# Kernel tuning notes

Measured on AMD Instinct MI355X. Metric: run time of the kernel, lower is better.

Reference implementation:

```python
import jax, jax.numpy as jnp
import numpy as np

# norse default LIFParameters / LIParameters constants
DT = 1e-3
TAU_SYN_INV = 200.0
TAU_MEM_INV = 100.0
V_LEAK = 0.0
V_TH = 1.0
V_RESET = 0.0
ALPHA = 100.0  # superspike surrogate-gradient slope


@jax.custom_vjp
def superspike(x):
    return (x > 0).astype(x.dtype)

def _ss_fwd(x):
    return (x > 0).astype(x.dtype), x

def _ss_bwd(x, g):
    return (g / (ALPHA * jnp.abs(x) + 1.0) ** 2,)

superspike.defvjp(_ss_fwd, _ss_bwd)


def lif_step(state, inp):
    """norse lif_feed_forward_step: decay v/i, spike on old current, then inject input."""
    v, i = state
    v_dec = v + DT * TAU_MEM_INV * ((V_LEAK - v) + i)
    i_dec = i - DT * TAU_SYN_INV * i
    z = superspike(v_dec - V_TH)
    v_new = (1.0 - z) * v_dec + z * V_RESET
    return z, (v_new, i_dec + inp)


def li_step(state, inp):
    """norse li_feed_forward_step: leaky integrator, output is the membrane voltage."""
    v, i = state
    v_new = v + DT * TAU_MEM_INV * ((V_LEAK - v) + i)
    i_new = i - DT * TAU_SYN_INV * i + inp
    return v_new, (v_new, i_new)


def setup_inputs() -> dict:
    key = jax.random.key(0)
    ks = jax.random.split(key, 5)
    B = 65536
    x = jax.random.normal(ks[0], (B, 1, 10, 10), dtype=jnp.float32)
    conv_w = jax.random.normal(ks[1], (2, 1, 4, 4), dtype=jnp.float32) * 0.3
    conv_b = jax.random.normal(ks[2], (2,), dtype=jnp.float32) * 0.1
    fc_w = jax.random.normal(ks[3], (10, 72), dtype=jnp.float32) * 0.1
    fc_b = jax.random.normal(ks[4], (10,), dtype=jnp.float32) * 0.1
    return {"x": x, "conv_w": conv_w, "conv_b": conv_b, "fc_w": fc_w, "fc_b": fc_b, "num_steps": 64}


def reference(x, conv_w, conv_b, fc_w, fc_b, num_steps):
    B = x.shape[0]
    out_dim = fc_w.shape[0]
    # static input: conv(x) identical at every step, hoist out of the time loop
    g = jax.lax.conv_general_dilated(
        x, conv_w, (1, 1), "VALID",
        dimension_numbers=("NCHW", "OIHW", "NCHW"),
    ) + conv_b[None, :, None, None]  # [B,2,7,7]

    def pool(z):  # MaxPool2d(kernel=2, stride=1), VALID
        return jax.lax.reduce_window(
            z, -jnp.inf, jax.lax.max, (1, 1, 2, 2), (1, 1, 1, 1), "VALID")

    s_lif0 = (jnp.zeros_like(g), jnp.zeros_like(g))                 # [B,2,7,7]
    s_li1_0 = (jnp.zeros((B, 2, 6, 6), x.dtype), jnp.zeros((B, 2, 6, 6), x.dtype))
    s_li2_0 = (jnp.zeros((B, out_dim), x.dtype), jnp.zeros((B, out_dim), x.dtype))

    def step(carry, _):
        s_lif, s1, s2 = carry
        z, s_lif = lif_step(s_lif, g)          # spikes [B,2,7,7]
        z = pool(z)                            # [B,2,6,6]
        z, s1 = li_step(s1, z)                 # LI voltage [B,2,6,6]
        z = z.reshape(B, -1)                   # [B,72]
        z = z @ fc_w.T + fc_b                  # [B,10]
        v, s2 = li_step(s2, z)                 # readout voltage [B,10]
        return (s_lif, s1, s2), None

    (s_lif, s1, s2), _ = jax.lax.scan(step, (s_lif0, s_li1_0, s_li2_0), None, length=num_steps)
    return s2[0]  # final readout membrane voltage [B, output_size]
```

## Files before the change

### kernel.cpp

```cpp
#include <hip/hip_runtime.h>

#define TMAX 64

__global__ __launch_bounds__(256) void snn_fused(
    const float* __restrict__ x,
    const float* __restrict__ conv_w,
    const float* __restrict__ conv_b,
    const float* __restrict__ fc_w,
    const float* __restrict__ fc_b,
    const int*   __restrict__ nsteps,
    float*       __restrict__ out,
    int B)
{
    __shared__ double d_F[TMAX];
    __shared__ float  s_r[TMAX];
    __shared__ float  s_tab[8][256];
    __shared__ float  s_fcw[720];
    __shared__ float  s_fcb[16];
    __shared__ float  s_cb;

    const int tid = threadIdx.x;
    int T = nsteps[0];
    if (T > TMAX) T = TMAX;
    if (T < 0) T = 0;

    if (tid < TMAX) {
        double p9 = 1.0, p8 = 1.0;
        for (int k = 0; k < tid; ++k) { p9 *= 0.9; p8 *= 0.8; }
        d_F[tid] = p9 - p8;
    }
    for (int idx = tid; idx < 720; idx += 256) s_fcw[idx] = fc_w[idx];
    if (tid < 10) s_fcb[tid] = fc_b[tid];
    __syncthreads();

    if (tid < TMAX) {
        double r = 0.0;
        if (tid < T) {
            const int n = T - 1 - tid;
            for (int u = 0; u <= n; ++u) r += d_F[n - u] * d_F[u];
        }
        s_r[tid] = (float)r;
    }
    if (tid == 0) {
        double cb = 0.0;
        for (int m = 0; m < T; ++m) cb += d_F[m];
        s_cb = (float)cb;
    }
    __syncthreads();

    {
        const int v8 = tid;
        #pragma unroll
        for (int k = 0; k < 8; ++k) {
            float ssum = 0.f;
            #pragma unroll
            for (int bb = 0; bb < 8; ++bb)
                if ((v8 >> bb) & 1) ssum += s_r[k * 8 + bb];
            s_tab[k][v8] = ssum;
        }
    }
    __syncthreads();

    const float cbsum = s_cb;

    const int gt = blockIdx.x * 256 + tid;
    const int b = gt >> 1;
    const int c = gt & 1;
    if (b >= B) return;

    const float* xb = x + b * 100;

    float wc[16];
    {
        const float4* wq = reinterpret_cast<const float4*>(conv_w + c * 16);
        #pragma unroll
        for (int k = 0; k < 4; ++k) {
            float4 t = wq[k];
            wc[4*k+0] = t.x; wc[4*k+1] = t.y; wc[4*k+2] = t.z; wc[4*k+3] = t.w;
        }
    }
    const float cbias = conv_b[c];

    float outacc[10];
    #pragma unroll
    for (int o = 0; o < 10; ++o) outacc[o] = 0.f;

    unsigned int plo[7], phi[7];
    #pragma unroll
    for (int xx = 0; xx < 7; ++xx) { plo[xx] = 0u; phi[xx] = 0u; }

    const int tlo = T < 32 ? T : 32;
    const int thi = T > 32 ? (T - 32) : 0;

    for (int y = 0; y < 7; ++y) {
        float gg7[7];
        #pragma unroll
        for (int xx = 0; xx < 7; ++xx) gg7[xx] = 0.f;
        #pragma unroll
        for (int ky = 0; ky < 4; ++ky) {
            float xrow[10];
            const float2* q = reinterpret_cast<const float2*>(xb + (y + ky) * 10);
            #pragma unroll
            for (int k = 0; k < 5; ++k) { float2 t = q[k]; xrow[2*k] = t.x; xrow[2*k+1] = t.y; }
            #pragma unroll
            for (int xx = 0; xx < 7; ++xx) {
                float a = gg7[xx];
                #pragma unroll
                for (int kx = 0; kx < 4; ++kx)
                    a = __fadd_rn(a, __fmul_rn(wc[ky*4 + kx], xrow[xx + kx]));
                gg7[xx] = a;
            }
        }
        #pragma unroll
        for (int xx = 0; xx < 7; ++xx) gg7[xx] = __fadd_rn(gg7[xx], cbias);

        float v[7], ii[7];
        unsigned int mlo[7], mhi[7];
        #pragma unroll
        for (int xx = 0; xx < 7; ++xx) { v[xx] = 0.f; ii[xx] = 0.f; mlo[xx] = 0u; mhi[xx] = 0u; }

        #pragma unroll 4
        for (int t = 0; t < tlo; ++t) {
            const unsigned int bit = 1u << t;
            #pragma unroll
            for (int xx = 0; xx < 7; ++xx) {
                const float imv  = __fsub_rn(ii[xx], v[xx]);
                const float vdec = __fadd_rn(v[xx], __fmul_rn(0.1f, imv));
                const float idec = __fsub_rn(ii[xx], __fmul_rn(0.2f, ii[xx]));
                const bool  sp   = vdec > 1.0f;
                v[xx]  = sp ? 0.f : vdec;
                ii[xx] = __fadd_rn(idec, gg7[xx]);
                if (sp) mlo[xx] |= bit;
            }
        }
        #pragma unroll 4
        for (int t = 0; t < thi; ++t) {
            const unsigned int bit = 1u << t;
            #pragma unroll
            for (int xx = 0; xx < 7; ++xx) {
                const float imv  = __fsub_rn(ii[xx], v[xx]);
                const float vdec = __fadd_rn(v[xx], __fmul_rn(0.1f, imv));
                const float idec = __fsub_rn(ii[xx], __fmul_rn(0.2f, ii[xx]));
                const bool  sp   = vdec > 1.0f;
                v[xx]  = sp ? 0.f : vdec;
                ii[xx] = __fadd_rn(idec, gg7[xx]);
                if (sp) mhi[xx] |= bit;
            }
        }

        if (y > 0) {
            const int jbase = c * 36 + (y - 1) * 6;
            #pragma unroll
            for (int px = 0; px < 6; ++px) {
                const unsigned int pl = plo[px] | plo[px+1] | mlo[px] | mlo[px+1];
                const unsigned int ph = phi[px] | phi[px+1] | mhi[px] | mhi[px+1];
                float a = s_tab[0][pl & 255] + s_tab[1][(pl >> 8) & 255]
                        + s_tab[2][(pl >> 16) & 255] + s_tab[3][pl >> 24]
                        + s_tab[4][ph & 255] + s_tab[5][(ph >> 8) & 255]
                        + s_tab[6][(ph >> 16) & 255] + s_tab[7][ph >> 24];
                const int j = jbase + px;
                #pragma unroll
                for (int o = 0; o < 10; ++o)
                    outacc[o] = fmaf(s_fcw[o * 72 + j], a, outacc[o]);
            }
        }
        #pragma unroll
        for (int xx = 0; xx < 7; ++xx) { plo[xx] = mlo[xx]; phi[xx] = mhi[xx]; }
    }

    #pragma unroll
    for (int o = 0; o < 10; ++o) {
        float tot = outacc[o] + __shfl_xor(outacc[o], 1);
        tot = fmaf(cbsum, s_fcb[o], tot);
        if (c == 0) out[b * 10 + o] = tot;
    }
}

extern "C" void kernel_launch(void* const* d_in, const int* in_sizes, int n_in,
                              void* d_out, int out_size, void* d_ws, size_t ws_size,
                              hipStream_t stream) {
    const float* x      = (const float*)d_in[0];
    const float* conv_w = (const float*)d_in[1];
    const float* conv_b = (const float*)d_in[2];
    const float* fc_w   = (const float*)d_in[3];
    const float* fc_b   = (const float*)d_in[4];
    const int*   nsteps = (const int*)d_in[5];
    float* outp = (float*)d_out;

    const int B = in_sizes[0] / 100;
    const int total = 2 * B;
    const int block = 256;
    const int grid = (total + block - 1) / block;
    snn_fused<<<grid, block, 0, stream>>>(x, conv_w, conv_b, fc_w, fc_b, nsteps, outp, B);
}
```

Measured before the change: 96.45 us.

## Split rows across two threads per channel and use carry-shift spike masks

Each (batch, channel) pair is now handled by two threads that each simulate four overlapping rows, doubling thread count at the cost of recomputing one shared row. Spike bitmasks are built with inline asm that shifts in the compare carry, removing per-step bit construction. The pooled-weight lookup table is reversed to match the new bit order. The partial sums are reduced across four lanes with shuffles.

Result: faster. 91.05 us (-5.6%).

```diff
diff --git a/kernel.cpp b/kernel.cpp
--- a/kernel.cpp
+++ b/kernel.cpp
@@ -14,6 +14,7 @@
 {
     __shared__ double d_F[TMAX];
     __shared__ float  s_r[TMAX];
+    __shared__ float  s_rb[TMAX];
     __shared__ float  s_tab[8][256];
     __shared__ float  s_fcw[720];
     __shared__ float  s_fcb[16];
@@ -23,6 +24,8 @@
     int T = nsteps[0];
     if (T > TMAX) T = TMAX;
     if (T < 0) T = 0;
+    const int tlo = T < 32 ? T : 32;
+    const int thi = T > 32 ? (T - 32) : 0;
 
     if (tid < TMAX) {
         double p9 = 1.0, p8 = 1.0;
@@ -48,6 +51,14 @@
     }
     __syncthreads();
 
+    if (tid < 32) {
+        s_rb[tid] = (tid < tlo) ? s_r[tlo - 1 - tid] : 0.f;
+    } else if (tid < 64) {
+        const int p = tid - 32;
+        s_rb[tid] = (p < thi) ? s_r[tlo + thi - 1 - p] : 0.f;
+    }
+    __syncthreads();
+
     {
         const int v8 = tid;
         #pragma unroll
@@ -55,7 +66,7 @@
             float ssum = 0.f;
             #pragma unroll
             for (int bb = 0; bb < 8; ++bb)
-                if ((v8 >> bb) & 1) ssum += s_r[k * 8 + bb];
+                if ((v8 >> bb) & 1) ssum += s_rb[k * 8 + bb];
             s_tab[k][v8] = ssum;
         }
     }
@@ -64,8 +75,9 @@
     const float cbsum = s_cb;
 
     const int gt = blockIdx.x * 256 + tid;
-    const int b = gt >> 1;
-    const int c = gt & 1;
+    const int h = gt & 1;
+    const int c = (gt >> 1) & 1;
+    const int b = gt >> 2;
     if (b >= B) return;
 
     const float* xb = x + b * 100;
@@ -86,13 +98,13 @@
     for (int o = 0; o < 10; ++o) outacc[o] = 0.f;
 
     unsigned int plo[7], phi[7];
-    #pragma unroll
-    for (int xx = 0; xx < 7; ++xx) { plo[xx] = 0u; phi[xx] = 0u; }
-
-    const int tlo = T < 32 ? T : 32;
-    const int thi = T > 32 ? (T - 32) : 0;
-
-    for (int y = 0; y < 7; ++y) {
+    float fzero = 0.0f;
+
+    const int ybase = 3 * h;
+
+    for (int r = 0; r < 4; ++r) {
+        const int y = ybase + r;
+
         float gg7[7];
         #pragma unroll
         for (int xx = 0; xx < 7; ++xx) gg7[xx] = 0.f;
@@ -121,35 +133,44 @@
 
         #pragma unroll 4
         for (int t = 0; t < tlo; ++t) {
-            const unsigned int bit = 1u << t;
             #pragma unroll
             for (int xx = 0; xx < 7; ++xx) {
                 const float imv  = __fsub_rn(ii[xx], v[xx]);
                 const float vdec = __fadd_rn(v[xx], __fmul_rn(0.1f, imv));
                 const float idec = __fsub_rn(ii[xx], __fmul_rn(0.2f, ii[xx]));
-                const bool  sp   = vdec > 1.0f;
-                v[xx]  = sp ? 0.f : vdec;
+                float vnew;
+                asm("v_cmp_lt_f32 vcc, 1.0, %[vd]\n\t"
+                    "v_cndmask_b32 %[vn], %[vd], %[vz], vcc\n\t"
+                    "v_addc_co_u32 %[mm], vcc, %[mm], %[mm], vcc"
+                    : [vn]"=v"(vnew), [mm]"+v"(mlo[xx])
+                    : [vd]"v"(vdec), [vz]"v"(fzero)
+                    : "vcc");
+                v[xx]  = vnew;
                 ii[xx] = __fadd_rn(idec, gg7[xx]);
-                if (sp) mlo[xx] |= bit;
             }
         }
         #pragma unroll 4
         for (int t = 0; t < thi; ++t) {
-            const unsigned int bit = 1u << t;
             #pragma unroll
             for (int xx = 0; xx < 7; ++xx) {
                 const float imv  = __fsub_rn(ii[xx], v[xx]);
                 const float vdec = __fadd_rn(v[xx], __fmul_rn(0.1f, imv));
                 const float idec = __fsub_rn(ii[xx], __fmul_rn(0.2f, ii[xx]));
-                const bool  sp   = vdec > 1.0f;
-                v[xx]  = sp ? 0.f : vdec;
+                float vnew;
+                asm("v_cmp_lt_f32 vcc, 1.0, %[vd]\n\t"
+                    "v_cndmask_b32 %[vn], %[vd], %[vz], vcc\n\t"
+                    "v_addc_co_u32 %[mm], vcc, %[mm], %[mm], vcc"
+                    : [vn]"=v"(vnew), [mm]"+v"(mhi[xx])
+                    : [vd]"v"(vdec), [vz]"v"(fzero)
+                    : "vcc");
+                v[xx]  = vnew;
                 ii[xx] = __fadd_rn(idec, gg7[xx]);
-                if (sp) mhi[xx] |= bit;
-            }
-        }
-
-        if (y > 0) {
-            const int jbase = c * 36 + (y - 1) * 6;
+            }
+        }
+
+        if (r > 0) {
+            const int py = ybase + r - 1;
+            const int jbase = c * 36 + py * 6;
             #pragma unroll
             for (int px = 0; px < 6; ++px) {
                 const unsigned int pl = plo[px] | plo[px+1] | mlo[px] | mlo[px+1];
@@ -170,9 +191,10 @@
 
     #pragma unroll
     for (int o = 0; o < 10; ++o) {
-        float tot = outacc[o] + __shfl_xor(outacc[o], 1);
+        float t1  = outacc[o] + __shfl_xor(outacc[o], 1);
+        float tot = t1 + __shfl_xor(t1, 2);
         tot = fmaf(cbsum, s_fcb[o], tot);
-        if (c == 0) out[b * 10 + o] = tot;
+        if ((gt & 3) == 0) out[b * 10 + o] = tot;
     }
 }
 
@@ -188,7 +210,7 @@
     float* outp = (float*)d_out;
 
     const int B = in_sizes[0] / 100;
-    const int total = 2 * B;
+    const int total = 4 * B;
     const int block = 256;
     const int grid = (total + block - 1) / block;
     snn_fused<<<grid, block, 0, stream>>>(x, conv_w, conv_b, fc_w, fc_b, nsteps, outp, B);
```
